# Performance work log

Measured on AMD Instinct MI355X. Metric: run time of the kernel, lower is better.

The kernel has to match this reference:

```python
import jax, jax.numpy as jnp
import numpy as np

# Standard MediaPipe FaceMesh lips landmark indices (40 points), as in the source repo.
LIPS_IDX = np.array([
    61, 185, 40, 39, 37, 0, 267, 269, 270, 409,
    291, 146, 91, 181, 84, 17, 314, 405, 321, 375,
    78, 191, 80, 81, 82, 13, 312, 311, 310, 415,
    95, 88, 178, 87, 14, 317, 402, 318, 324, 308,
], dtype=np.int32)

NORMALIZED_LENGTH = 64  # init arg
N_LM = 2 * 21 + 40      # 82 gathered landmarks


def setup_inputs() -> dict:
    key = jax.random.key(0)
    frames = jax.random.normal(key, (32768, 543, 3), dtype=jnp.float32)
    return {"frames": frames}


def reference(frames):
    L = NORMALIZED_LENGTH
    xy = frames[:, :, :2]                      # [T, 543, 2]
    lh = xy[:, 468:489]                        # [T, 21, 2]
    rh = xy[:, 522:543]                        # [T, 21, 2]
    lips = xy[:, LIPS_IDX]                     # [T, 40, 2]
    raw = jnp.concatenate([lh, rh, lips], axis=1)  # [T, 82, 2]
    T = raw.shape[0]

    # Segment boundaries: linspace(0, T-1, L+1) cast to int; segment i = [b[i], b[i+1])
    boundaries = jnp.linspace(0.0, float(T - 1), L + 1).astype(jnp.int32)
    t = jnp.arange(T, dtype=jnp.int32)
    # seg[t] = largest i with boundaries[i] <= t; t >= b[L] maps to L (dropped)
    seg = jnp.searchsorted(boundaries, t, side='right').astype(jnp.int32) - 1

    valid = ~jnp.isnan(raw)
    vf = valid.astype(raw.dtype)
    x0 = jnp.where(valid, raw, jnp.zeros_like(raw))

    cnt = jax.ops.segment_sum(vf, seg, num_segments=L + 1)[:L]   # [L, 82, 2]
    s1 = jax.ops.segment_sum(x0, seg, num_segments=L + 1)[:L]    # [L, 82, 2]
    mean = s1 / cnt                                              # nan if empty segment

    # nan-std: sqrt of nan-mean of squared deviations (two-pass, faithful)
    mean_full = jnp.concatenate([mean, jnp.zeros((1, N_LM, 2), mean.dtype)], axis=0)
    dev = jnp.where(valid, raw - mean_full[seg], jnp.zeros_like(raw))
    s2 = jax.ops.segment_sum(dev * dev, seg, num_segments=L + 1)[:L]
    std = jnp.sqrt(s2 / cnt)

    stats = jnp.concatenate([mean, std], axis=1)                 # [L, 164, 2]
    feats = jnp.where(jnp.isnan(stats), jnp.zeros_like(stats), stats)
    return feats.reshape(L, 2 * 2 * N_LM)                        # [L, 328]
```

## Files before the change

### kernel.cpp

```cpp
#include <hip/hip_runtime.h>
#include <hip/hip_bf16.h>

#define N_SEG 64
#define N_LMK 82
#define N_P   164
#define N_CHUNK 16
#define ROW 1629

__device__ __constant__ int LIPS[40] = {
    61, 185, 40, 39, 37, 0, 267, 269, 270, 409, 291, 146, 91, 181, 84, 17,
    314, 405, 321, 375, 78, 191, 80, 81, 82, 13, 312, 311, 310, 415, 95, 88,
    178, 87, 14, 317, 402, 318, 324, 308};

__global__ __launch_bounds__(192) void accum_kernel(
    const float* __restrict__ frames, float* __restrict__ ws, int T) {
    const int s   = blockIdx.x;
    const int kc  = blockIdx.y;
    const int tid = threadIdx.x;
    if (tid >= N_P) return;

    const int l = tid >> 1;
    const int c = tid & 1;
    int lm;
    if (l < 21)      lm = 468 + l;
    else if (l < 42) lm = 501 + l;
    else             lm = LIPS[l - 42];
    const int off = lm * 3 + c;

    const float step = (float)(T - 1) / 64.0f;
    const int lo = (int)((float)s * step);
    const int hi = (int)((float)(s + 1) * step);

    float sum = 0.f, sq = 0.f, cnt = 0.f;
    for (int f = lo + kc; f < hi; f += N_CHUNK) {
        float v = frames[(size_t)f * ROW + off];
        if (v == v) {
            sum += v;
            sq  += v * v;
            cnt += 1.f;
        }
    }
    const int idx = s * N_P + tid;
    atomicAdd(&ws[idx],               sum);
    atomicAdd(&ws[N_SEG * N_P + idx], sq);
    atomicAdd(&ws[2 * N_SEG * N_P + idx], cnt);
}

__global__ __launch_bounds__(256) void finalize_kernel(
    const float* __restrict__ ws, float* __restrict__ out) {
    const int i = blockIdx.x * blockDim.x + threadIdx.x;
    if (i >= N_SEG * N_P) return;
    const int s = i / N_P;
    const int p = i % N_P;

    const float s1  = ws[i];
    const float s2  = ws[N_SEG * N_P + i];
    const float cnt = ws[2 * N_SEG * N_P + i];

    float mean = s1 / cnt;
    float var  = fmaxf(s2 / cnt - mean * mean, 0.f);
    float sd   = sqrtf(var);
    if (!(mean == mean)) mean = 0.f;
    if (!(sd == sd))     sd   = 0.f;

    out[s * 328 + p]       = mean;
    out[s * 328 + 164 + p] = sd;
}

extern "C" void kernel_launch(void* const* d_in, const int* in_sizes, int n_in,
                              void* d_out, int out_size, void* d_ws, size_t ws_size,
                              hipStream_t stream) {
    const float* frames = (const float*)d_in[0];
    float* out = (float*)d_out;
    float* ws  = (float*)d_ws;
    const int T = in_sizes[0] / ROW;

    hipMemsetAsync(ws, 0, 3 * N_SEG * N_P * sizeof(float), stream);

    dim3 grid(N_SEG, N_CHUNK);
    accum_kernel<<<grid, 192, 0, stream>>>(frames, ws, T);

    finalize_kernel<<<(N_SEG * N_P + 255) / 256, 256, 0, stream>>>(ws, out);
}
```

Baseline: 27.63 us.

## Replace atomic accumulation with per-chunk partial sums and unroll frame loop

After: 25.05 us. 9.3% less time.

```diff
diff --git a/kernel.cpp b/kernel.cpp
--- a/kernel.cpp
+++ b/kernel.cpp
@@ -2,51 +2,126 @@
 #include <hip/hip_bf16.h>
 
 #define N_SEG 64
-#define N_LMK 82
 #define N_P   164
-#define N_CHUNK 16
-#define ROW 1629
+#define ROW   1629
+#define N_CHUNK 32
+#define N_CHUNK_AT 16
 
 __device__ __constant__ int LIPS[40] = {
     61, 185, 40, 39, 37, 0, 267, 269, 270, 409, 291, 146, 91, 181, 84, 17,
     314, 405, 321, 375, 78, 191, 80, 81, 82, 13, 312, 311, 310, 415, 95, 88,
     178, 87, 14, 317, 402, 318, 324, 308};
 
-__global__ __launch_bounds__(192) void accum_kernel(
+__device__ __forceinline__ int landmark_offset(int tid) {
+    const int l = tid >> 1;
+    const int c = tid & 1;
+    int lm;
+    if (l < 21)      lm = 468 + l;
+    else if (l < 42) lm = 501 + l;
+    else             lm = LIPS[l - 42];
+    return lm * 3 + c;
+}
+
+__device__ __forceinline__ void seg_bounds(int s, int T, int* lo, int* hi) {
+    const float step = (float)(T - 1) / 64.0f;
+    *lo = (int)((float)s * step);
+    *hi = (int)((float)(s + 1) * step);
+}
+
+__global__ __launch_bounds__(192) void accum_part(
     const float* __restrict__ frames, float* __restrict__ ws, int T) {
     const int s   = blockIdx.x;
     const int kc  = blockIdx.y;
     const int tid = threadIdx.x;
     if (tid >= N_P) return;
 
-    const int l = tid >> 1;
-    const int c = tid & 1;
-    int lm;
-    if (l < 21)      lm = 468 + l;
-    else if (l < 42) lm = 501 + l;
-    else             lm = LIPS[l - 42];
-    const int off = lm * 3 + c;
-
-    const float step = (float)(T - 1) / 64.0f;
-    const int lo = (int)((float)s * step);
-    const int hi = (int)((float)(s + 1) * step);
+    const int off = landmark_offset(tid);
+    int lo, hi;
+    seg_bounds(s, T, &lo, &hi);
 
     float sum = 0.f, sq = 0.f, cnt = 0.f;
-    for (int f = lo + kc; f < hi; f += N_CHUNK) {
+    int f = lo + kc;
+    for (; f + 3 * N_CHUNK < hi; f += 4 * N_CHUNK) {
+        float v0 = frames[(size_t)f * ROW + off];
+        float v1 = frames[(size_t)(f + N_CHUNK) * ROW + off];
+        float v2 = frames[(size_t)(f + 2 * N_CHUNK) * ROW + off];
+        float v3 = frames[(size_t)(f + 3 * N_CHUNK) * ROW + off];
+        if (v0 == v0) { sum += v0; sq = fmaf(v0, v0, sq); cnt += 1.f; }
+        if (v1 == v1) { sum += v1; sq = fmaf(v1, v1, sq); cnt += 1.f; }
+        if (v2 == v2) { sum += v2; sq = fmaf(v2, v2, sq); cnt += 1.f; }
+        if (v3 == v3) { sum += v3; sq = fmaf(v3, v3, sq); cnt += 1.f; }
+    }
+    for (; f < hi; f += N_CHUNK) {
         float v = frames[(size_t)f * ROW + off];
-        if (v == v) {
-            sum += v;
-            sq  += v * v;
-            cnt += 1.f;
-        }
+        if (v == v) { sum += v; sq = fmaf(v, v, sq); cnt += 1.f; }
     }
+
+    const size_t base = ((size_t)(s * N_CHUNK + kc) * N_P + tid) * 3;
+    ws[base]     = sum;
+    ws[base + 1] = sq;
+    ws[base + 2] = cnt;
+}
+
+__global__ __launch_bounds__(256) void finalize_part(
+    const float* __restrict__ ws, float* __restrict__ out) {
+    const int i = blockIdx.x * blockDim.x + threadIdx.x;
+    if (i >= N_SEG * N_P) return;
+    const int s = i / N_P;
+    const int p = i % N_P;
+
+    float s1 = 0.f, s2 = 0.f, c = 0.f;
+    for (int kc = 0; kc < N_CHUNK; ++kc) {
+        const size_t base = ((size_t)(s * N_CHUNK + kc) * N_P + p) * 3;
+        s1 += ws[base];
+        s2 += ws[base + 1];
+        c  += ws[base + 2];
+    }
+
+    float mean = s1 / c;
+    float var  = fmaxf(s2 / c - mean * mean, 0.f);
+    float sd   = sqrtf(var);
+    if (!(mean == mean)) mean = 0.f;
+    if (!(sd == sd))     sd   = 0.f;
+
+    out[s * 328 + p]       = mean;
+    out[s * 328 + 164 + p] = sd;
+}
+
+__global__ __launch_bounds__(192) void accum_atomic(
+    const float* __restrict__ frames, float* __restrict__ ws, int T) {
+    const int s   = blockIdx.x;
+    const int kc  = blockIdx.y;
+    const int tid = threadIdx.x;
+    if (tid >= N_P) return;
+
+    const int off = landmark_offset(tid);
+    int lo, hi;
+    seg_bounds(s, T, &lo, &hi);
+
+    float sum = 0.f, sq = 0.f, cnt = 0.f;
+    int f = lo + kc;
+    for (; f + 3 * N_CHUNK_AT < hi; f += 4 * N_CHUNK_AT) {
+        float v0 = frames[(size_t)f * ROW + off];
+        float v1 = frames[(size_t)(f + N_CHUNK_AT) * ROW + off];
+        float v2 = frames[(size_t)(f + 2 * N_CHUNK_AT) * ROW + off];
+        float v3 = frames[(size_t)(f + 3 * N_CHUNK_AT) * ROW + off];
+        if (v0 == v0) { sum += v0; sq = fmaf(v0, v0, sq); cnt += 1.f; }
+        if (v1 == v1) { sum += v1; sq = fmaf(v1, v1, sq); cnt += 1.f; }
+        if (v2 == v2) { sum += v2; sq = fmaf(v2, v2, sq); cnt += 1.f; }
+        if (v3 == v3) { sum += v3; sq = fmaf(v3, v3, sq); cnt += 1.f; }
+    }
+    for (; f < hi; f += N_CHUNK_AT) {
+        float v = frames[(size_t)f * ROW + off];
+        if (v == v) { sum += v; sq = fmaf(v, v, sq); cnt += 1.f; }
+    }
+
     const int idx = s * N_P + tid;
-    atomicAdd(&ws[idx],               sum);
-    atomicAdd(&ws[N_SEG * N_P + idx], sq);
+    atomicAdd(&ws[idx],                 sum);
+    atomicAdd(&ws[N_SEG * N_P + idx],   sq);
     atomicAdd(&ws[2 * N_SEG * N_P + idx], cnt);
 }
 
-__global__ __launch_bounds__(256) void finalize_kernel(
+__global__ __launch_bounds__(256) void finalize_atomic(
     const float* __restrict__ ws, float* __restrict__ out) {
     const int i = blockIdx.x * blockDim.x + threadIdx.x;
     if (i >= N_SEG * N_P) return;
@@ -55,10 +130,10 @@
 
     const float s1  = ws[i];
     const float s2  = ws[N_SEG * N_P + i];
-    const float cnt = ws[2 * N_SEG * N_P + i];
+    const float c   = ws[2 * N_SEG * N_P + i];
 
-    float mean = s1 / cnt;
-    float var  = fmaxf(s2 / cnt - mean * mean, 0.f);
+    float mean = s1 / c;
+    float var  = fmaxf(s2 / c - mean * mean, 0.f);
     float sd   = sqrtf(var);
     if (!(mean == mean)) mean = 0.f;
     if (!(sd == sd))     sd   = 0.f;
@@ -75,10 +150,16 @@
     float* ws  = (float*)d_ws;
     const int T = in_sizes[0] / ROW;
 
-    hipMemsetAsync(ws, 0, 3 * N_SEG * N_P * sizeof(float), stream);
+    const size_t need = (size_t)N_SEG * N_CHUNK * N_P * 3 * sizeof(float);
 
-    dim3 grid(N_SEG, N_CHUNK);
-    accum_kernel<<<grid, 192, 0, stream>>>(frames, ws, T);
-
-    finalize_kernel<<<(N_SEG * N_P + 255) / 256, 256, 0, stream>>>(ws, out);
+    if (ws_size >= need) {
+        dim3 grid(N_SEG, N_CHUNK);
+        accum_part<<<grid, 192, 0, stream>>>(frames, ws, T);
+        finalize_part<<<(N_SEG * N_P + 255) / 256, 256, 0, stream>>>(ws, out);
+    } else {
+        hipMemsetAsync(ws, 0, 3 * N_SEG * N_P * sizeof(float), stream);
+        dim3 grid(N_SEG, N_CHUNK_AT);
+        accum_atomic<<<grid, 192, 0, stream>>>(frames, ws, T);
+        finalize_atomic<<<(N_SEG * N_P + 255) / 256, 256, 0, stream>>>(ws, out);
+    }
 }
```
